# Optimization experiments

Hardware: AMD Instinct MI355X
Metric: run time of the kernel (lower is better)

## Reference

```python
import jax, jax.numpy as jnp
import numpy as np

E, S = 32768, 16
H, D_IN, EDGE_IN = 128, 128, 16
N_SRC, N_DST = 20000, 5000
HEADS, LAYERS, NUM_CLASS = 8, 2, 10
DH = H // HEADS


def _layer_norm(x, g, b, eps=1e-5):
    mu = jnp.mean(x, axis=-1, keepdims=True)
    var = jnp.mean((x - mu) ** 2, axis=-1, keepdims=True)
    return (x - mu) * jax.lax.rsqrt(var + eps) * g + b


def _encoder(e, e_mask, Wqkv, bqkv, Wo, bo, ln1_g, ln1_b, W1, b1, W2, b2, ln2_g, ln2_b):
    # e: [E,S,H]; e_mask: [E,S], True = padding. Post-norm encoder (PyTorch default).
    neg = jnp.float32(-1e9)
    for l in range(LAYERS):
        qkv = e @ Wqkv[l] + bqkv[l]                      # [E,S,3H]
        q, k, v = jnp.split(qkv, 3, axis=-1)
        q = q.reshape(E, S, HEADS, DH)
        k = k.reshape(E, S, HEADS, DH)
        v = v.reshape(E, S, HEADS, DH)
        scores = jnp.einsum('eqhd,ekhd->ehqk', q, k) / np.float32(np.sqrt(DH))
        scores = jnp.where(e_mask[:, None, None, :], neg, scores)
        attn = jax.nn.softmax(scores, axis=-1)
        ctx = jnp.einsum('ehqk,ekhd->eqhd', attn, v).reshape(E, S, H)
        e = _layer_norm(e + (ctx @ Wo[l] + bo[l]), ln1_g[l], ln1_b[l])
        ff = jax.nn.relu(e @ W1[l] + b1[l]) @ W2[l] + b2[l]
        e = _layer_norm(e + ff, ln2_g[l], ln2_b[l])
    return e


def _forward(node_features, edge_features, seq_times, subg_norm,
             W_ein, b_ein, enc_Wqkv, enc_bqkv, enc_Wo, enc_bo, enc_ln1_g, enc_ln1_b,
             enc_W1, enc_b1, enc_W2, enc_b2, enc_ln2_g, enc_ln2_b,
             W_eout, b_eout, W_node, b_node, W_fc, b_fc,
             e_len, e_mask, src_ids, dst_ids, layer_nid):
    h = node_features                                             # [N_src, D_IN]
    self_h = h[layer_nid]                                         # [N_dst, D_IN]
    self_h_tmp = jnp.concatenate([self_h, jnp.zeros((N_DST, H), h.dtype)], axis=1) @ W_eout + b_eout
    # message_func: per-edge sequence -> embed -> transformer -> pool -> concat with src h
    e = jnp.concatenate([edge_features, seq_times[..., None]], axis=-1)  # [E,S,EDGE_IN]
    e = jax.nn.relu(e @ W_ein + b_ein)                                   # [E,S,H]
    e = _encoder(e, e_mask, enc_Wqkv, enc_bqkv, enc_Wo, enc_bo,
                 enc_ln1_g, enc_ln1_b, enc_W1, enc_b1, enc_W2, enc_b2, enc_ln2_g, enc_ln2_b)
    valid = (~e_mask).astype(e.dtype)[..., None]
    e = jnp.sum(e * valid, axis=1) / e_len.astype(e.dtype)[:, None]      # masked mean pool [E,H]
    m = jax.nn.relu(jnp.concatenate([h[src_ids], e], axis=1) @ W_eout + b_eout)  # [E,H]
    h_agg = jax.ops.segment_sum(m, dst_ids, num_segments=N_DST)          # ragged mailbox sum
    hh = (h_agg - self_h_tmp) * subg_norm                                # NodeUpdate (train branch)
    z = jax.nn.relu(jnp.concatenate([self_h, hh], axis=1) @ W_node + b_node)
    return z @ W_fc + b_fc                                               # [N_dst, NUM_CLASS]


def setup_inputs() -> dict:
    key = jax.random.key(0)
    ks = jax.random.split(key, 32)
    inp = {}
    inp['node_features'] = jax.random.normal(ks[0], (N_SRC, D_IN), jnp.float32)
    inp['edge_features'] = jax.random.normal(ks[1], (E, S, EDGE_IN - 1), jnp.float32)
    inp['seq_times'] = jax.random.uniform(ks[2], (E, S), jnp.float32)
    e_len = jax.random.randint(ks[3], (E,), 1, S + 1).astype(jnp.int32)
    inp['e_len'] = e_len
    inp['e_mask'] = jnp.arange(S, dtype=jnp.int32)[None, :] >= e_len[:, None]  # True = pad
    inp['src_ids'] = jax.random.randint(ks[4], (E,), 0, N_SRC).astype(jnp.int32)
    inp['dst_ids'] = jax.random.randint(ks[5], (E,), 0, N_DST).astype(jnp.int32)
    inp['layer_nid'] = jax.random.randint(ks[6], (N_DST,), 0, N_SRC).astype(jnp.int32)
    inp['subg_norm'] = jax.random.uniform(ks[7], (N_DST, 1), jnp.float32, minval=0.01, maxval=1.0)

    def lin(k, fi, fo):
        return jax.random.normal(k, (fi, fo), jnp.float32) / np.float32(np.sqrt(fi))

    inp['W_ein'] = lin(ks[8], EDGE_IN, H); inp['b_ein'] = jnp.zeros((H,), jnp.float32)
    inp['enc_Wqkv'] = jax.random.normal(ks[9], (LAYERS, H, 3 * H), jnp.float32) / np.float32(np.sqrt(H))
    inp['enc_bqkv'] = jnp.zeros((LAYERS, 3 * H), jnp.float32)
    inp['enc_Wo'] = jax.random.normal(ks[10], (LAYERS, H, H), jnp.float32) / np.float32(np.sqrt(H))
    inp['enc_bo'] = jnp.zeros((LAYERS, H), jnp.float32)
    inp['enc_ln1_g'] = jnp.ones((LAYERS, H), jnp.float32); inp['enc_ln1_b'] = jnp.zeros((LAYERS, H), jnp.float32)
    inp['enc_W1'] = jax.random.normal(ks[11], (LAYERS, H, H), jnp.float32) / np.float32(np.sqrt(H))
    inp['enc_b1'] = jnp.zeros((LAYERS, H), jnp.float32)
    inp['enc_W2'] = jax.random.normal(ks[12], (LAYERS, H, H), jnp.float32) / np.float32(np.sqrt(H))
    inp['enc_b2'] = jnp.zeros((LAYERS, H), jnp.float32)
    inp['enc_ln2_g'] = jnp.ones((LAYERS, H), jnp.float32); inp['enc_ln2_b'] = jnp.zeros((LAYERS, H), jnp.float32)
    inp['W_eout'] = lin(ks[13], D_IN + H, H); inp['b_eout'] = jnp.zeros((H,), jnp.float32)
    inp['W_node'] = lin(ks[14], D_IN + H, H); inp['b_node'] = jnp.zeros((H,), jnp.float32)
    inp['W_fc'] = lin(ks[15], H, NUM_CLASS); inp['b_fc'] = jnp.zeros((NUM_CLASS,), jnp.float32)
    return inp


def reference(node_features, edge_features, seq_times, e_len, e_mask, src_ids, dst_ids,
              layer_nid, subg_norm, W_ein, b_ein, enc_Wqkv, enc_bqkv, enc_Wo, enc_bo,
              enc_ln1_g, enc_ln1_b, enc_W1, enc_b1, enc_W2, enc_b2, enc_ln2_g, enc_ln2_b,
              W_eout, b_eout, W_node, b_node, W_fc, b_fc):
    return _forward(node_features, edge_features, seq_times, subg_norm,
                    W_ein, b_ein, enc_Wqkv, enc_bqkv, enc_Wo, enc_bo, enc_ln1_g, enc_ln1_b,
                    enc_W1, enc_b1, enc_W2, enc_b2, enc_ln2_g, enc_ln2_b,
                    W_eout, b_eout, W_node, b_node, W_fc, b_fc,
                    e_len, e_mask, src_ids, dst_ids, layer_nid)
```

## Files before the change

### kernel.cpp

```cpp
#include <hip/hip_runtime.h>

typedef __attribute__((ext_vector_type(8))) short bf16x8;
typedef __attribute__((ext_vector_type(4))) float f32x4;

#define E_N      32768
#define N_DST_N  5000
#define NCLS     10

#define OFF_HAGG   0
#define OFF_POOL   2560000
#define OFF_WPACK  10948608

#define PK_QKV(l)  ((l) * 6144)
#define PK_WO(l)   (12288 + (l) * 2048)
#define PK_W1(l)   (16384 + (l) * 2048)
#define PK_W2(l)   (20480 + (l) * 2048)
#define PK_WEOUT   24576

#define QP 408
#define AP 136
#define EP 132

__device__ __forceinline__ unsigned short f2bf(float f) {
    unsigned int u = __float_as_uint(f);
    u += 0x7fffu + ((u >> 16) & 1u);
    return (unsigned short)(u >> 16);
}
__device__ __forceinline__ float bf2f(unsigned short u) {
    return __uint_as_float(((unsigned int)u) << 16);
}

__global__ void pack_weights(const float* __restrict__ Wqkv,
                             const float* __restrict__ Wo,
                             const float* __restrict__ W1,
                             const float* __restrict__ W2,
                             const float* __restrict__ W_eout,
                             unsigned short* __restrict__ wpack) {
    int gid = blockIdx.x * 256 + threadIdx.x;
    if (gid >= 229376) return;
    int id = gid;
    const float* src; int K, N, li;
    if (id < 98304)       { src = Wqkv + (id / 49152) * 49152; li = id % 49152; K = 128; N = 384; }
    else if (id < 131072) { id -= 98304;  src = Wo + (id / 16384) * 16384; li = id % 16384; K = 128; N = 128; }
    else if (id < 163840) { id -= 131072; src = W1 + (id / 16384) * 16384; li = id % 16384; K = 128; N = 128; }
    else if (id < 196608) { id -= 163840; src = W2 + (id / 16384) * 16384; li = id % 16384; K = 128; N = 128; }
    else                  { li = id - 196608; src = W_eout; K = 256; N = 128; }
    int j = li & 7, lane = (li >> 3) & 63, rest = li >> 9;
    int ks = K >> 5;
    int kk = rest % ks, t = rest / ks;
    int k = kk * 32 + ((lane >> 4) << 3) + j;
    int n = t * 16 + (lane & 15);
    wpack[gid] = f2bf(src[k * N + n]);
}

__global__ __launch_bounds__(256, 3) void edge_kernel(
    const float* __restrict__ edge_features,
    const float* __restrict__ seq_times,
    const int*   __restrict__ e_len,
    const float* __restrict__ W_ein, const float* __restrict__ b_ein,
    const float* __restrict__ bqkv,  const float* __restrict__ bo,
    const float* __restrict__ ln1_g, const float* __restrict__ ln1_b,
    const float* __restrict__ b1,    const float* __restrict__ b2,
    const float* __restrict__ ln2_g, const float* __restrict__ ln2_b,
    const unsigned short* __restrict__ wpack,
    unsigned short* __restrict__ pooled)
{
    __shared__ float e_f32[32][EP];
    __shared__ __align__(16) unsigned short a_bf[32][AP];
    __shared__ __align__(16) unsigned short qkv_bf[32][QP];
    __shared__ float x_lds[32][16];

    const int tid  = threadIdx.x;
    const int e0   = blockIdx.x * 2;
    const int lane = tid & 63;
    const int w    = tid >> 6;
    const int c16  = lane & 15;
    const int row4 = (lane >> 4) << 2;
    const int kblk = (lane >> 4) << 3;
    const int len0 = e_len[e0];
    const int len1 = e_len[e0 + 1];

#pragma unroll
    for (int idx = tid; idx < 512; idx += 256) {
        int e = idx >> 8, s = (idx >> 4) & 15, i = idx & 15;
        x_lds[e * 16 + s][i] = (i < 15) ? edge_features[(e0 + e) * 240 + s * 15 + i]
                                        : seq_times[(e0 + e) * 16 + s];
    }
    __syncthreads();

    {
        int c = tid & 127, er = (tid >> 7) * 16;
        float acc[16];
#pragma unroll
        for (int r = 0; r < 16; ++r) acc[r] = 0.f;
#pragma unroll
        for (int i = 0; i < 16; ++i) {
            float wt = W_ein[i * 128 + c];
#pragma unroll
            for (int r = 0; r < 16; ++r)
                acc[r] = fmaf(x_lds[er + r][i], wt, acc[r]);
        }
        float bv = b_ein[c];
#pragma unroll
        for (int r = 0; r < 16; ++r) {
            float v = fmaxf(acc[r] + bv, 0.f);
            e_f32[er + r][c] = v;
            a_bf[er + r][c]  = f2bf(v);
        }
    }
    __syncthreads();

    const bf16x8* WP = (const bf16x8*)wpack;

    for (int l = 0; l < 2; ++l) {
        {
            bf16x8 af[2][4];
#pragma unroll
            for (int rt = 0; rt < 2; ++rt)
#pragma unroll
                for (int kk = 0; kk < 4; ++kk)
                    af[rt][kk] = *(const bf16x8*)&a_bf[rt * 16 + c16][kk * 32 + kblk];
            const bf16x8* B = WP + PK_QKV(l);
#pragma unroll
            for (int half = 0; half < 2; ++half) {
                bf16x8 bq[3][4];
#pragma unroll
                for (int ti = 0; ti < 3; ++ti)
#pragma unroll
                    for (int kk = 0; kk < 4; ++kk)
                        bq[ti][kk] = B[((w * 6 + half * 3 + ti) * 4 + kk) * 64 + lane];
#pragma unroll
                for (int ti = 0; ti < 3; ++ti) {
                    int t = w * 6 + half * 3 + ti;
                    int seg = t >> 3;
                    int ldcol = seg * 136 + (t & 7) * 16 + c16;
                    float bias = bqkv[l * 384 + t * 16 + c16];
#pragma unroll
                    for (int rt = 0; rt < 2; ++rt) {
                        f32x4 acc = {0.f, 0.f, 0.f, 0.f};
#pragma unroll
                        for (int kk = 0; kk < 4; ++kk)
                            acc = __builtin_amdgcn_mfma_f32_16x16x32_bf16(
                                af[rt][kk], bq[ti][kk], acc, 0, 0, 0);
#pragma unroll
                        for (int r = 0; r < 4; ++r)
                            qkv_bf[rt * 16 + row4 + r][ldcol] = f2bf(acc[r] + bias);
                    }
                }
            }
        }
        __syncthreads();

        {
            int e  = tid >> 7;
            int hb = ((tid >> 4) & 7) * 16;
            int qq = tid & 15;
            int er = e * 16;
            int len = e ? len1 : len0;
            float qv[16];
            {
                bf16x8 v0 = *(const bf16x8*)&qkv_bf[er + qq][hb];
                bf16x8 v1 = *(const bf16x8*)&qkv_bf[er + qq][hb + 8];
#pragma unroll
                for (int j = 0; j < 8; ++j) {
                    qv[j]     = bf2f((unsigned short)v0[j]);
                    qv[8 + j] = bf2f((unsigned short)v1[j]);
                }
            }
            float sc[16];
            float mx = -1e30f;
#pragma unroll
            for (int kk = 0; kk < 16; ++kk) {
                bf16x8 k0 = *(const bf16x8*)&qkv_bf[er + kk][136 + hb];
                bf16x8 k1 = *(const bf16x8*)&qkv_bf[er + kk][136 + hb + 8];
                float s = 0.f;
#pragma unroll
                for (int j = 0; j < 8; ++j) {
                    s = fmaf(qv[j],     bf2f((unsigned short)k0[j]), s);
                    s = fmaf(qv[8 + j], bf2f((unsigned short)k1[j]), s);
                }
                s *= 0.25f;
                sc[kk] = s;
                mx = fmaxf(mx, (kk < len) ? s : -1e30f);
            }
            float sum = 0.f;
#pragma unroll
            for (int kk = 0; kk < 16; ++kk) {
                float p = (kk < len) ? __expf(sc[kk] - mx) : 0.f;
                sc[kk] = p;
                sum += p;
            }
            float inv = 1.f / sum;
            float ctx[16];
#pragma unroll
            for (int d = 0; d < 16; ++d) ctx[d] = 0.f;
#pragma unroll
            for (int kk = 0; kk < 16; ++kk) {
                float p = sc[kk] * inv;
                bf16x8 v0 = *(const bf16x8*)&qkv_bf[er + kk][272 + hb];
                bf16x8 v1 = *(const bf16x8*)&qkv_bf[er + kk][272 + hb + 8];
#pragma unroll
                for (int j = 0; j < 8; ++j) {
                    ctx[j]     = fmaf(p, bf2f((unsigned short)v0[j]), ctx[j]);
                    ctx[8 + j] = fmaf(p, bf2f((unsigned short)v1[j]), ctx[8 + j]);
                }
            }
            bf16x8 o0, o1;
#pragma unroll
            for (int j = 0; j < 8; ++j) {
                o0[j] = (short)f2bf(ctx[j]);
                o1[j] = (short)f2bf(ctx[8 + j]);
            }
            __syncthreads();
            *(bf16x8*)&a_bf[er + qq][hb]     = o0;
            *(bf16x8*)&a_bf[er + qq][hb + 8] = o1;
        }
        __syncthreads();

        {
            bf16x8 af[2][4];
#pragma unroll
            for (int rt = 0; rt < 2; ++rt)
#pragma unroll
                for (int kk = 0; kk < 4; ++kk)
                    af[rt][kk] = *(const bf16x8*)&a_bf[rt * 16 + c16][kk * 32 + kblk];
            const bf16x8* B = WP + PK_WO(l);
            bf16x8 bw[2][4];
#pragma unroll
            for (int ti = 0; ti < 2; ++ti)
#pragma unroll
                for (int kk = 0; kk < 4; ++kk)
                    bw[ti][kk] = B[((w * 2 + ti) * 4 + kk) * 64 + lane];
#pragma unroll
            for (int ti = 0; ti < 2; ++ti) {
                int col = (w * 2 + ti) * 16 + c16;
                float bias = bo[l * 128 + col];
#pragma unroll
                for (int rt = 0; rt < 2; ++rt) {
                    f32x4 acc = {0.f, 0.f, 0.f, 0.f};
#pragma unroll
                    for (int kk = 0; kk < 4; ++kk)
                        acc = __builtin_amdgcn_mfma_f32_16x16x32_bf16(
                            af[rt][kk], bw[ti][kk], acc, 0, 0, 0);
#pragma unroll
                    for (int r = 0; r < 4; ++r)
                        e_f32[rt * 16 + row4 + r][col] += acc[r] + bias;
                }
            }
        }
        __syncthreads();

        {
            const float* g = ln1_g + l * 128;
            const float* b = ln1_b + l * 128;
            int r = tid >> 3, j = tid & 7;
            float vals[16];
#pragma unroll
            for (int m = 0; m < 16; ++m) vals[m] = e_f32[r][j + 8 * m];
            float s = 0.f;
#pragma unroll
            for (int m = 0; m < 16; ++m) s += vals[m];
            s += __shfl_xor(s, 1); s += __shfl_xor(s, 2); s += __shfl_xor(s, 4);
            float mu = s * (1.f / 128.f);
            float v = 0.f;
#pragma unroll
            for (int m = 0; m < 16; ++m) { float d = vals[m] - mu; v = fmaf(d, d, v); }
            v += __shfl_xor(v, 1); v += __shfl_xor(v, 2); v += __shfl_xor(v, 4);
            float inv = rsqrtf(v * (1.f / 128.f) + 1e-5f);
#pragma unroll
            for (int m = 0; m < 16; ++m) {
                int col = j + 8 * m;
                float y = (vals[m] - mu) * inv * g[col] + b[col];
                e_f32[r][col] = y;
                a_bf[r][col]  = f2bf(y);
            }
        }
        __syncthreads();

        {
            bf16x8 af[2][4];
#pragma unroll
            for (int rt = 0; rt < 2; ++rt)
#pragma unroll
                for (int kk = 0; kk < 4; ++kk)
                    af[rt][kk] = *(const bf16x8*)&a_bf[rt * 16 + c16][kk * 32 + kblk];
            const bf16x8* B = WP + PK_W1(l);
            bf16x8 bw[2][4];
#pragma unroll
            for (int ti = 0; ti < 2; ++ti)
#pragma unroll
                for (int kk = 0; kk < 4; ++kk)
                    bw[ti][kk] = B[((w * 2 + ti) * 4 + kk) * 64 + lane];
            f32x4 acc2[2][2];
#pragma unroll
            for (int ti = 0; ti < 2; ++ti)
#pragma unroll
                for (int rt = 0; rt < 2; ++rt) {
                    f32x4 acc = {0.f, 0.f, 0.f, 0.f};
#pragma unroll
                    for (int kk = 0; kk < 4; ++kk)
                        acc = __builtin_amdgcn_mfma_f32_16x16x32_bf16(
                            af[rt][kk], bw[ti][kk], acc, 0, 0, 0);
                    acc2[ti][rt] = acc;
                }
            __syncthreads();
#pragma unroll
            for (int ti = 0; ti < 2; ++ti) {
                int col = (w * 2 + ti) * 16 + c16;
                float bias = b1[l * 128 + col];
#pragma unroll
                for (int rt = 0; rt < 2; ++rt)
#pragma unroll
                    for (int r = 0; r < 4; ++r)
                        a_bf[rt * 16 + row4 + r][col] =
                            f2bf(fmaxf(acc2[ti][rt][r] + bias, 0.f));
            }
        }
        __syncthreads();

        {
            bf16x8 af[2][4];
#pragma unroll
            for (int rt = 0; rt < 2; ++rt)
#pragma unroll
                for (int kk = 0; kk < 4; ++kk)
                    af[rt][kk] = *(const bf16x8*)&a_bf[rt * 16 + c16][kk * 32 + kblk];
            const bf16x8* B = WP + PK_W2(l);
            bf16x8 bw[2][4];
#pragma unroll
            for (int ti = 0; ti < 2; ++ti)
#pragma unroll
                for (int kk = 0; kk < 4; ++kk)
                    bw[ti][kk] = B[((w * 2 + ti) * 4 + kk) * 64 + lane];
#pragma unroll
            for (int ti = 0; ti < 2; ++ti) {
                int col = (w * 2 + ti) * 16 + c16;
                float bias = b2[l * 128 + col];
#pragma unroll
                for (int rt = 0; rt < 2; ++rt) {
                    f32x4 acc = {0.f, 0.f, 0.f, 0.f};
#pragma unroll
                    for (int kk = 0; kk < 4; ++kk)
                        acc = __builtin_amdgcn_mfma_f32_16x16x32_bf16(
                            af[rt][kk], bw[ti][kk], acc, 0, 0, 0);
#pragma unroll
                    for (int r = 0; r < 4; ++r)
                        e_f32[rt * 16 + row4 + r][col] += acc[r] + bias;
                }
            }
        }
        __syncthreads();

        {
            const float* g = ln2_g + l * 128;
            const float* b = ln2_b + l * 128;
            int r = tid >> 3, j = tid & 7;
            float vals[16];
#pragma unroll
            for (int m = 0; m < 16; ++m) vals[m] = e_f32[r][j + 8 * m];
            float s = 0.f;
#pragma unroll
            for (int m = 0; m < 16; ++m) s += vals[m];
            s += __shfl_xor(s, 1); s += __shfl_xor(s, 2); s += __shfl_xor(s, 4);
            float mu = s * (1.f / 128.f);
            float v = 0.f;
#pragma unroll
            for (int m = 0; m < 16; ++m) { float d = vals[m] - mu; v = fmaf(d, d, v); }
            v += __shfl_xor(v, 1); v += __shfl_xor(v, 2); v += __shfl_xor(v, 4);
            float inv = rsqrtf(v * (1.f / 128.f) + 1e-5f);
#pragma unroll
            for (int m = 0; m < 16; ++m) {
                int col = j + 8 * m;
                float y = (vals[m] - mu) * inv * g[col] + b[col];
                e_f32[r][col] = y;
                a_bf[r][col]  = f2bf(y);
            }
        }
        __syncthreads();
    }

    {
        int e = tid >> 7, c = tid & 127;
        int len = e ? len1 : len0;
        float s = 0.f;
#pragma unroll
        for (int ss = 0; ss < 16; ++ss)
            s += (ss < len) ? e_f32[e * 16 + ss][c] : 0.f;
        pooled[(e0 + e) * 128 + c] = f2bf(s / (float)len);
    }
}

__global__ __launch_bounds__(256) void edge_out_kernel(
    const float* __restrict__ node_features,
    const int* __restrict__ src_ids, const int* __restrict__ dst_ids,
    const unsigned short* __restrict__ pooled,
    const unsigned short* __restrict__ wpack,
    const float* __restrict__ b_eout,
    float* __restrict__ h_agg)
{
    __shared__ __align__(16) unsigned short a2[16][264];
    __shared__ int dst_s[16];
    const int tid = threadIdx.x, lane = tid & 63, w = tid >> 6;
    const int e0 = blockIdx.x * 16;

    {
        int r = tid >> 4, cm = tid & 15;
        int e = e0 + r;
        int src = src_ids[e];
#pragma unroll
        for (int m = 0; m < 8; ++m) {
            int col = cm + 16 * m;
            a2[r][col] = f2bf(node_features[src * 128 + col]);
        }
#pragma unroll
        for (int m = 0; m < 8; ++m) {
            int col = cm + 16 * m;
            a2[r][128 + col] = pooled[e * 128 + col];
        }
        if (tid < 16) dst_s[tid] = dst_ids[e0 + tid];
    }
    __syncthreads();

    const int c16 = lane & 15, row4 = (lane >> 4) << 2, kblk = (lane >> 4) << 3;
    bf16x8 af[8];
#pragma unroll
    for (int kk = 0; kk < 8; ++kk)
        af[kk] = *(const bf16x8*)&a2[c16][kk * 32 + kblk];
    const bf16x8* B = (const bf16x8*)wpack + PK_WEOUT;
#pragma unroll
    for (int ti = 0; ti < 2; ++ti) {
        int t = w * 2 + ti;
        f32x4 acc = {0.f, 0.f, 0.f, 0.f};
#pragma unroll
        for (int kk = 0; kk < 8; ++kk)
            acc = __builtin_amdgcn_mfma_f32_16x16x32_bf16(
                af[kk], B[(t * 8 + kk) * 64 + lane], acc, 0, 0, 0);
        int col = t * 16 + c16;
        float bias = b_eout[col];
#pragma unroll
        for (int r = 0; r < 4; ++r) {
            int row = row4 + r;
            float v = fmaxf(acc[r] + bias, 0.f);
            atomicAdd(&h_agg[dst_s[row] * 128 + col], v);
        }
    }
}

__global__ __launch_bounds__(128) void node_kernel(
    const float* __restrict__ node_features,
    const int*   __restrict__ layer_nid,
    const float* __restrict__ subg_norm,
    const float* __restrict__ h_agg,
    const float* __restrict__ W_eout, const float* __restrict__ b_eout,
    const float* __restrict__ W_node, const float* __restrict__ b_node,
    const float* __restrict__ W_fc,   const float* __restrict__ b_fc,
    float* __restrict__ out)
{
    __shared__ float sh[128];
    __shared__ float hh[128];
    __shared__ float z[128];

    const int n   = blockIdx.x;
    const int tid = threadIdx.x;
    const int nid = layer_nid[n];
    const float norm = subg_norm[n];

    sh[tid] = node_features[nid * 128 + tid];
    __syncthreads();

    float acc = 0.f;
#pragma unroll 4
    for (int k = 0; k < 128; ++k)
        acc = fmaf(sh[k], W_eout[k * 128 + tid], acc);
    acc += b_eout[tid];
    hh[tid] = (h_agg[n * 128 + tid] - acc) * norm;
    __syncthreads();

    float za = 0.f;
#pragma unroll 4
    for (int k = 0; k < 128; ++k)
        za = fmaf(sh[k], W_node[k * 128 + tid], za);
#pragma unroll 4
    for (int k = 0; k < 128; ++k)
        za = fmaf(hh[k], W_node[(128 + k) * 128 + tid], za);
    za += b_node[tid];
    z[tid] = fmaxf(za, 0.f);
    __syncthreads();

    if (tid < NCLS) {
        float o = 0.f;
#pragma unroll 4
        for (int k = 0; k < 128; ++k)
            o = fmaf(z[k], W_fc[k * NCLS + tid], o);
        out[n * NCLS + tid] = o + b_fc[tid];
    }
}


extern "C" void kernel_launch(void* const* d_in, const int* in_sizes, int n_in,
                              void* d_out, int out_size, void* d_ws, size_t ws_size,
                              hipStream_t stream) {
    const float* node_features = (const float*)d_in[0];
    const float* edge_features = (const float*)d_in[1];
    const float* seq_times     = (const float*)d_in[2];
    const int*   e_len         = (const int*)d_in[3];
    const int*   src_ids       = (const int*)d_in[5];
    const int*   dst_ids       = (const int*)d_in[6];
    const int*   layer_nid     = (const int*)d_in[7];
    const float* subg_norm     = (const float*)d_in[8];
    const float* W_ein  = (const float*)d_in[9];
    const float* b_ein  = (const float*)d_in[10];
    const float* Wqkv   = (const float*)d_in[11];
    const float* bqkv   = (const float*)d_in[12];
    const float* Wo     = (const float*)d_in[13];
    const float* bo     = (const float*)d_in[14];
    const float* ln1_g  = (const float*)d_in[15];
    const float* ln1_b  = (const float*)d_in[16];
    const float* W1     = (const float*)d_in[17];
    const float* b1     = (const float*)d_in[18];
    const float* W2     = (const float*)d_in[19];
    const float* b2     = (const float*)d_in[20];
    const float* ln2_g  = (const float*)d_in[21];
    const float* ln2_b  = (const float*)d_in[22];
    const float* W_eout = (const float*)d_in[23];
    const float* b_eout = (const float*)d_in[24];
    const float* W_node = (const float*)d_in[25];
    const float* b_node = (const float*)d_in[26];
    const float* W_fc   = (const float*)d_in[27];
    const float* b_fc   = (const float*)d_in[28];

    float*          h_agg  = (float*)((char*)d_ws + OFF_HAGG);
    unsigned short* pooled = (unsigned short*)((char*)d_ws + OFF_POOL);
    unsigned short* wpack  = (unsigned short*)((char*)d_ws + OFF_WPACK);

    pack_weights<<<896, 256, 0, stream>>>(Wqkv, Wo, W1, W2, W_eout, wpack);
    hipMemsetAsync(h_agg, 0, (size_t)N_DST_N * 128 * sizeof(float), stream);

    edge_kernel<<<E_N / 2, 256, 0, stream>>>(
        edge_features, seq_times, e_len,
        W_ein, b_ein, bqkv, bo, ln1_g, ln1_b, b1, b2, ln2_g, ln2_b,
        wpack, pooled);

    edge_out_kernel<<<E_N / 16, 256, 0, stream>>>(
        node_features, src_ids, dst_ids, pooled, wpack, b_eout, h_agg);

    node_kernel<<<N_DST_N, 128, 0, stream>>>(
        node_features, layer_nid, subg_norm, h_agg,
        W_eout, b_eout, W_node, b_node, W_fc, b_fc, (float*)d_out);
}
```

Baseline: 888.5 us.

## Move edge encoder attention and input projection to MFMA, keep residual in registers

The per-edge encoder kernel now computes the input embedding and both attention products (QK^T and PV) with bf16 MFMA instructions instead of scalar FMA loops. It stores V transposed and K separately in LDS, and keeps the fp32 residual stream in registers rather than an LDS fp32 buffer. LayerNorm becomes a register-based two-pass reduction through small LDS partial-sum arrays, and mean pooling reads directly from registers. The intent is less LDS traffic and capacity, fewer barriers and scalar FLOPs, and higher occupancy. In exchange, attention probabilities and the input are rounded to bf16, variance uses E[x^2]-mu^2, and half the lanes in the attention MFMAs carry zero padding.

```diff
diff --git a/kernel.cpp b/kernel.cpp
--- a/kernel.cpp
+++ b/kernel.cpp
@@ -1,6 +1,7 @@
 #include <hip/hip_runtime.h>
 
 typedef __attribute__((ext_vector_type(8))) short bf16x8;
+typedef __attribute__((ext_vector_type(4))) short s16x4;
 typedef __attribute__((ext_vector_type(4))) float f32x4;
 
 #define E_N      32768
@@ -16,18 +17,12 @@
 #define PK_W1(l)   (16384 + (l) * 2048)
 #define PK_W2(l)   (20480 + (l) * 2048)
 #define PK_WEOUT   24576
-
-#define QP 408
-#define AP 136
-#define EP 132
+#define PK_WEIN    28672
 
 __device__ __forceinline__ unsigned short f2bf(float f) {
     unsigned int u = __float_as_uint(f);
     u += 0x7fffu + ((u >> 16) & 1u);
     return (unsigned short)(u >> 16);
-}
-__device__ __forceinline__ float bf2f(unsigned short u) {
-    return __uint_as_float(((unsigned int)u) << 16);
 }
 
 __global__ void pack_weights(const float* __restrict__ Wqkv,
@@ -35,9 +30,18 @@
                              const float* __restrict__ W1,
                              const float* __restrict__ W2,
                              const float* __restrict__ W_eout,
+                             const float* __restrict__ W_ein,
                              unsigned short* __restrict__ wpack) {
     int gid = blockIdx.x * 256 + threadIdx.x;
-    if (gid >= 229376) return;
+    if (gid >= 233472) return;
+    if (gid >= 229376) {
+        int li = gid - 229376;
+        int j = li & 7, lane = (li >> 3) & 63, t = li >> 9;
+        int k = ((lane >> 4) << 3) + j;
+        int n = t * 16 + (lane & 15);
+        wpack[gid] = (k < 16) ? f2bf(W_ein[k * 128 + n]) : (unsigned short)0;
+        return;
+    }
     int id = gid;
     const float* src; int K, N, li;
     if (id < 98304)       { src = Wqkv + (id / 49152) * 49152; li = id % 49152; K = 128; N = 384; }
@@ -53,11 +57,65 @@
     wpack[gid] = f2bf(src[k * N + n]);
 }
 
+__device__ __forceinline__ void layer_norm_reg(
+    float res[2][2][4],
+    const float gcol[2], const float bcol[2],
+    unsigned short (*a_bf)[136],
+    float (*psum)[4], float (*psq)[4],
+    int w, int c16, int row4)
+{
+    float sv[2][4], qv[2][4];
+#pragma unroll
+    for (int rt = 0; rt < 2; ++rt)
+#pragma unroll
+        for (int r = 0; r < 4; ++r) {
+            float x0 = res[rt][0][r], x1 = res[rt][1][r];
+            float s = x0 + x1;
+            float q = x0 * x0 + x1 * x1;
+#pragma unroll
+            for (int d = 1; d < 16; d <<= 1) {
+                s += __shfl_xor(s, d);
+                q += __shfl_xor(q, d);
+            }
+            sv[rt][r] = s; qv[rt][r] = q;
+        }
+    if (c16 == 0) {
+#pragma unroll
+        for (int rt = 0; rt < 2; ++rt)
+#pragma unroll
+            for (int r = 0; r < 4; ++r) {
+                int row = rt * 16 + row4 + r;
+                psum[row][w] = sv[rt][r];
+                psq[row][w]  = qv[rt][r];
+            }
+    }
+    __syncthreads();
+#pragma unroll
+    for (int rt = 0; rt < 2; ++rt)
+#pragma unroll
+        for (int r = 0; r < 4; ++r) {
+            int row = rt * 16 + row4 + r;
+            float4 S = *(const float4*)&psum[row][0];
+            float4 Q = *(const float4*)&psq[row][0];
+            float sum = (S.x + S.y) + (S.z + S.w);
+            float sq  = (Q.x + Q.y) + (Q.z + Q.w);
+            float mu  = sum * (1.f / 128.f);
+            float var = sq * (1.f / 128.f) - mu * mu;
+            float inv = rsqrtf(var + 1e-5f);
+#pragma unroll
+            for (int ti = 0; ti < 2; ++ti) {
+                float y = (res[rt][ti][r] - mu) * inv * gcol[ti] + bcol[ti];
+                res[rt][ti][r] = y;
+                a_bf[row][w * 32 + ti * 16 + c16] = f2bf(y);
+            }
+        }
+}
+
 __global__ __launch_bounds__(256, 3) void edge_kernel(
     const float* __restrict__ edge_features,
     const float* __restrict__ seq_times,
     const int*   __restrict__ e_len,
-    const float* __restrict__ W_ein, const float* __restrict__ b_ein,
+    const float* __restrict__ b_ein,
     const float* __restrict__ bqkv,  const float* __restrict__ bo,
     const float* __restrict__ ln1_g, const float* __restrict__ ln1_b,
     const float* __restrict__ b1,    const float* __restrict__ b2,
@@ -65,52 +123,74 @@
     const unsigned short* __restrict__ wpack,
     unsigned short* __restrict__ pooled)
 {
-    __shared__ float e_f32[32][EP];
-    __shared__ __align__(16) unsigned short a_bf[32][AP];
-    __shared__ __align__(16) unsigned short qkv_bf[32][QP];
-    __shared__ float x_lds[32][16];
+    __shared__ __align__(16) unsigned short a_bf[32][136];
+    __shared__ __align__(16) unsigned short k_bf[32][136];
+    __shared__ __align__(16) unsigned short vT[2][128][24];
+    __shared__ __align__(16) unsigned short x_bf[32][40];
+    __shared__ __align__(16) float psum[32][4];
+    __shared__ __align__(16) float psq[32][4];
 
     const int tid  = threadIdx.x;
     const int e0   = blockIdx.x * 2;
     const int lane = tid & 63;
     const int w    = tid >> 6;
     const int c16  = lane & 15;
-    const int row4 = (lane >> 4) << 2;
-    const int kblk = (lane >> 4) << 3;
+    const int g    = lane >> 4;
+    const int row4 = g << 2;
+    const int kblk = g << 3;
     const int len0 = e_len[e0];
     const int len1 = e_len[e0 + 1];
-
-#pragma unroll
-    for (int idx = tid; idx < 512; idx += 256) {
-        int e = idx >> 8, s = (idx >> 4) & 15, i = idx & 15;
-        x_lds[e * 16 + s][i] = (i < 15) ? edge_features[(e0 + e) * 240 + s * 15 + i]
-                                        : seq_times[(e0 + e) * 16 + s];
-    }
-    __syncthreads();
+    const f32x4 z4 = {0.f, 0.f, 0.f, 0.f};
+
+    float res[2][2][4];
+
+    float lnG[2][2][2], lnB[2][2][2];
+#pragma unroll
+    for (int l = 0; l < 2; ++l)
+#pragma unroll
+        for (int ti = 0; ti < 2; ++ti) {
+            int col = w * 32 + ti * 16 + c16;
+            lnG[l][0][ti] = ln1_g[l * 128 + col];
+            lnB[l][0][ti] = ln1_b[l * 128 + col];
+            lnG[l][1][ti] = ln2_g[l * 128 + col];
+            lnB[l][1][ti] = ln2_b[l * 128 + col];
+        }
+
+    for (int idx = tid; idx < 1024; idx += 256) {
+        int r = idx >> 5, cc = idx & 31;
+        int e = r >> 4, s = r & 15;
+        float v = 0.f;
+        if (cc < 15)       v = edge_features[(e0 + e) * 240 + s * 15 + cc];
+        else if (cc == 15) v = seq_times[(e0 + e) * 16 + s];
+        x_bf[r][cc] = f2bf(v);
+    }
+    __syncthreads();
+
+    const bf16x8* WP = (const bf16x8*)wpack;
 
     {
-        int c = tid & 127, er = (tid >> 7) * 16;
-        float acc[16];
-#pragma unroll
-        for (int r = 0; r < 16; ++r) acc[r] = 0.f;
-#pragma unroll
-        for (int i = 0; i < 16; ++i) {
-            float wt = W_ein[i * 128 + c];
-#pragma unroll
-            for (int r = 0; r < 16; ++r)
-                acc[r] = fmaf(x_lds[er + r][i], wt, acc[r]);
-        }
-        float bv = b_ein[c];
-#pragma unroll
-        for (int r = 0; r < 16; ++r) {
-            float v = fmaxf(acc[r] + bv, 0.f);
-            e_f32[er + r][c] = v;
-            a_bf[er + r][c]  = f2bf(v);
-        }
-    }
-    __syncthreads();
-
-    const bf16x8* WP = (const bf16x8*)wpack;
+        bf16x8 axf[2];
+#pragma unroll
+        for (int rt = 0; rt < 2; ++rt)
+            axf[rt] = *(const bf16x8*)&x_bf[rt * 16 + c16][kblk];
+#pragma unroll
+        for (int ti = 0; ti < 2; ++ti) {
+            bf16x8 bw = WP[PK_WEIN + (2 * w + ti) * 64 + lane];
+            int col = (2 * w + ti) * 16 + c16;
+            float bias = b_ein[col];
+#pragma unroll
+            for (int rt = 0; rt < 2; ++rt) {
+                f32x4 acc = __builtin_amdgcn_mfma_f32_16x16x32_bf16(axf[rt], bw, z4, 0, 0, 0);
+#pragma unroll
+                for (int r = 0; r < 4; ++r) {
+                    float v = fmaxf(acc[r] + bias, 0.f);
+                    res[rt][ti][r] = v;
+                    a_bf[rt * 16 + row4 + r][col] = f2bf(v);
+                }
+            }
+        }
+    }
+    __syncthreads();
 
     for (int l = 0; l < 2; ++l) {
         {
@@ -120,100 +200,96 @@
 #pragma unroll
                 for (int kk = 0; kk < 4; ++kk)
                     af[rt][kk] = *(const bf16x8*)&a_bf[rt * 16 + c16][kk * 32 + kblk];
+            __syncthreads();
             const bf16x8* B = WP + PK_QKV(l);
 #pragma unroll
-            for (int half = 0; half < 2; ++half) {
-                bf16x8 bq[3][4];
-#pragma unroll
-                for (int ti = 0; ti < 3; ++ti)
+            for (int seg = 0; seg < 3; ++seg) {
+                bf16x8 bq[2][4];
+#pragma unroll
+                for (int ti = 0; ti < 2; ++ti)
 #pragma unroll
                     for (int kk = 0; kk < 4; ++kk)
-                        bq[ti][kk] = B[((w * 6 + half * 3 + ti) * 4 + kk) * 64 + lane];
-#pragma unroll
-                for (int ti = 0; ti < 3; ++ti) {
-                    int t = w * 6 + half * 3 + ti;
-                    int seg = t >> 3;
-                    int ldcol = seg * 136 + (t & 7) * 16 + c16;
-                    float bias = bqkv[l * 384 + t * 16 + c16];
+                        bq[ti][kk] = B[((seg * 8 + 2 * w + ti) * 4 + kk) * 64 + lane];
+#pragma unroll
+                for (int ti = 0; ti < 2; ++ti) {
+                    int col = (2 * w + ti) * 16 + c16;
+                    float bias = bqkv[l * 384 + seg * 128 + col];
 #pragma unroll
                     for (int rt = 0; rt < 2; ++rt) {
-                        f32x4 acc = {0.f, 0.f, 0.f, 0.f};
+                        f32x4 acc = z4;
 #pragma unroll
                         for (int kk = 0; kk < 4; ++kk)
                             acc = __builtin_amdgcn_mfma_f32_16x16x32_bf16(
                                 af[rt][kk], bq[ti][kk], acc, 0, 0, 0);
-#pragma unroll
-                        for (int r = 0; r < 4; ++r)
-                            qkv_bf[rt * 16 + row4 + r][ldcol] = f2bf(acc[r] + bias);
+                        if (seg == 0) {
+#pragma unroll
+                            for (int r = 0; r < 4; ++r)
+                                a_bf[rt * 16 + row4 + r][col] = f2bf(acc[r] + bias);
+                        } else if (seg == 1) {
+#pragma unroll
+                            for (int r = 0; r < 4; ++r)
+                                k_bf[rt * 16 + row4 + r][col] = f2bf(acc[r] + bias);
+                        } else {
+                            s16x4 pk;
+#pragma unroll
+                            for (int r = 0; r < 4; ++r)
+                                pk[r] = (short)f2bf(acc[r] + bias);
+                            *(s16x4*)&vT[rt][col][row4] = pk;
+                        }
                     }
                 }
             }
         }
         __syncthreads();
 
-        {
-            int e  = tid >> 7;
-            int hb = ((tid >> 4) & 7) * 16;
-            int qq = tid & 15;
+#pragma unroll
+        for (int i = 0; i < 4; ++i) {
+            int pp = w * 4 + i;
+            int e  = pp >> 3;
+            int hb = (pp & 7) * 16;
             int er = e * 16;
             int len = e ? len1 : len0;
-            float qv[16];
-            {
-                bf16x8 v0 = *(const bf16x8*)&qkv_bf[er + qq][hb];
-                bf16x8 v1 = *(const bf16x8*)&qkv_bf[er + qq][hb + 8];
-#pragma unroll
-                for (int j = 0; j < 8; ++j) {
-                    qv[j]     = bf2f((unsigned short)v0[j]);
-                    qv[8 + j] = bf2f((unsigned short)v1[j]);
-                }
-            }
-            float sc[16];
-            float mx = -1e30f;
-#pragma unroll
-            for (int kk = 0; kk < 16; ++kk) {
-                bf16x8 k0 = *(const bf16x8*)&qkv_bf[er + kk][136 + hb];
-                bf16x8 k1 = *(const bf16x8*)&qkv_bf[er + kk][136 + hb + 8];
-                float s = 0.f;
-#pragma unroll
-                for (int j = 0; j < 8; ++j) {
-                    s = fmaf(qv[j],     bf2f((unsigned short)k0[j]), s);
-                    s = fmaf(qv[8 + j], bf2f((unsigned short)k1[j]), s);
-                }
-                s *= 0.25f;
-                sc[kk] = s;
-                mx = fmaxf(mx, (kk < len) ? s : -1e30f);
-            }
-            float sum = 0.f;
-#pragma unroll
-            for (int kk = 0; kk < 16; ++kk) {
-                float p = (kk < len) ? __expf(sc[kk] - mx) : 0.f;
-                sc[kk] = p;
-                sum += p;
-            }
-            float inv = 1.f / sum;
-            float ctx[16];
-#pragma unroll
-            for (int d = 0; d < 16; ++d) ctx[d] = 0.f;
-#pragma unroll
-            for (int kk = 0; kk < 16; ++kk) {
-                float p = sc[kk] * inv;
-                bf16x8 v0 = *(const bf16x8*)&qkv_bf[er + kk][272 + hb];
-                bf16x8 v1 = *(const bf16x8*)&qkv_bf[er + kk][272 + hb + 8];
-#pragma unroll
-                for (int j = 0; j < 8; ++j) {
-                    ctx[j]     = fmaf(p, bf2f((unsigned short)v0[j]), ctx[j]);
-                    ctx[8 + j] = fmaf(p, bf2f((unsigned short)v1[j]), ctx[8 + j]);
-                }
-            }
-            bf16x8 o0, o1;
-#pragma unroll
-            for (int j = 0; j < 8; ++j) {
-                o0[j] = (short)f2bf(ctx[j]);
-                o1[j] = (short)f2bf(ctx[8 + j]);
-            }
-            __syncthreads();
-            *(bf16x8*)&a_bf[er + qq][hb]     = o0;
-            *(bf16x8*)&a_bf[er + qq][hb + 8] = o1;
+            bf16x8 kf = {0,0,0,0,0,0,0,0};
+            bf16x8 qf = {0,0,0,0,0,0,0,0};
+            bf16x8 vf = {0,0,0,0,0,0,0,0};
+            if (lane < 32) {
+                kf = *(const bf16x8*)&k_bf[er + c16][hb + kblk];
+                qf = *(const bf16x8*)&a_bf[er + c16][hb + kblk];
+                vf = *(const bf16x8*)&vT[e][hb + c16][kblk];
+            }
+            f32x4 st = __builtin_amdgcn_mfma_f32_16x16x32_bf16(kf, qf, z4, 0, 0, 0);
+            float sv[4]; float mx = -1e30f;
+#pragma unroll
+            for (int r = 0; r < 4; ++r) {
+                sv[r] = st[r] * 0.25f;
+                if (4 * g + r < len) mx = fmaxf(mx, sv[r]);
+            }
+            mx = fmaxf(mx, __shfl_xor(mx, 16));
+            mx = fmaxf(mx, __shfl_xor(mx, 32));
+            float p[4]; float sum = 0.f;
+#pragma unroll
+            for (int r = 0; r < 4; ++r) {
+                float pe = (4 * g + r < len) ? __expf(sv[r] - mx) : 0.f;
+                p[r] = pe; sum += pe;
+            }
+            sum += __shfl_xor(sum, 16);
+            sum += __shfl_xor(sum, 32);
+            float inv = __fdividef(1.f, sum);
+            unsigned int own0 = (unsigned int)f2bf(p[0] * inv) | ((unsigned int)f2bf(p[1] * inv) << 16);
+            unsigned int own1 = (unsigned int)f2bf(p[2] * inv) | ((unsigned int)f2bf(p[3] * inv) << 16);
+            unsigned int t0a = (unsigned int)__shfl((int)own0, (lane + 16) & 63);
+            unsigned int t1a = (unsigned int)__shfl((int)own1, (lane + 16) & 63);
+            unsigned int t0b = (unsigned int)__shfl((int)own0, (lane + 32) & 63);
+            unsigned int t1b = (unsigned int)__shfl((int)own1, (lane + 32) & 63);
+            union { unsigned int u[4]; bf16x8 v; } pb;
+            if (g == 0)      { pb.u[0] = own0; pb.u[1] = own1; pb.u[2] = t0a; pb.u[3] = t1a; }
+            else if (g == 1) { pb.u[0] = t0a;  pb.u[1] = t1a;  pb.u[2] = t0b; pb.u[3] = t1b; }
+            else             { pb.u[0] = 0; pb.u[1] = 0; pb.u[2] = 0; pb.u[3] = 0; }
+            f32x4 ct = __builtin_amdgcn_mfma_f32_16x16x32_bf16(vf, pb.v, z4, 0, 0, 0);
+            s16x4 cpk;
+#pragma unroll
+            for (int r = 0; r < 4; ++r) cpk[r] = (short)f2bf(ct[r]);
+            *(s16x4*)&a_bf[er + c16][hb + 4 * g] = cpk;
         }
         __syncthreads();
 
@@ -230,51 +306,25 @@
             for (int ti = 0; ti < 2; ++ti)
 #pragma unroll
                 for (int kk = 0; kk < 4; ++kk)
-                    bw[ti][kk] = B[((w * 2 + ti) * 4 + kk) * 64 + lane];
+                    bw[ti][kk] = B[((2 * w + ti) * 4 + kk) * 64 + lane];
 #pragma unroll
             for (int ti = 0; ti < 2; ++ti) {
-                int col = (w * 2 + ti) * 16 + c16;
+                int col = (2 * w + ti) * 16 + c16;
                 float bias = bo[l * 128 + col];
 #pragma unroll
                 for (int rt = 0; rt < 2; ++rt) {
-                    f32x4 acc = {0.f, 0.f, 0.f, 0.f};
+                    f32x4 acc = z4;
 #pragma unroll
                     for (int kk = 0; kk < 4; ++kk)
                         acc = __builtin_amdgcn_mfma_f32_16x16x32_bf16(
                             af[rt][kk], bw[ti][kk], acc, 0, 0, 0);
 #pragma unroll
                     for (int r = 0; r < 4; ++r)
-                        e_f32[rt * 16 + row4 + r][col] += acc[r] + bias;
+                        res[rt][ti][r] += acc[r] + bias;
                 }
             }
         }
-        __syncthreads();
-
-        {
-            const float* g = ln1_g + l * 128;
-            const float* b = ln1_b + l * 128;
-            int r = tid >> 3, j = tid & 7;
-            float vals[16];
-#pragma unroll
-            for (int m = 0; m < 16; ++m) vals[m] = e_f32[r][j + 8 * m];
-            float s = 0.f;
-#pragma unroll
-            for (int m = 0; m < 16; ++m) s += vals[m];
-            s += __shfl_xor(s, 1); s += __shfl_xor(s, 2); s += __shfl_xor(s, 4);
-            float mu = s * (1.f / 128.f);
-            float v = 0.f;
-#pragma unroll
-            for (int m = 0; m < 16; ++m) { float d = vals[m] - mu; v = fmaf(d, d, v); }
-            v += __shfl_xor(v, 1); v += __shfl_xor(v, 2); v += __shfl_xor(v, 4);
-            float inv = rsqrtf(v * (1.f / 128.f) + 1e-5f);
-#pragma unroll
-            for (int m = 0; m < 16; ++m) {
-                int col = j + 8 * m;
-                float y = (vals[m] - mu) * inv * g[col] + b[col];
-                e_f32[r][col] = y;
-                a_bf[r][col]  = f2bf(y);
-            }
-        }
+        layer_norm_reg(res, lnG[l][0], lnB[l][0], a_bf, psum, psq, w, c16, row4);
         __syncthreads();
 
         {
@@ -290,13 +340,13 @@
             for (int ti = 0; ti < 2; ++ti)
 #pragma unroll
                 for (int kk = 0; kk < 4; ++kk)
-                    bw[ti][kk] = B[((w * 2 + ti) * 4 + kk) * 64 + lane];
+                    bw[ti][kk] = B[((2 * w + ti) * 4 + kk) * 64 + lane];
             f32x4 acc2[2][2];
 #pragma unroll
             for (int ti = 0; ti < 2; ++ti)
 #pragma unroll
                 for (int rt = 0; rt < 2; ++rt) {
-                    f32x4 acc = {0.f, 0.f, 0.f, 0.f};
+                    f32x4 acc = z4;
 #pragma unroll
                     for (int kk = 0; kk < 4; ++kk)
                         acc = __builtin_amdgcn_mfma_f32_16x16x32_bf16(
@@ -306,7 +356,7 @@
             __syncthreads();
 #pragma unroll
             for (int ti = 0; ti < 2; ++ti) {
-                int col = (w * 2 + ti) * 16 + c16;
+                int col = (2 * w + ti) * 16 + c16;
                 float bias = b1[l * 128 + col];
 #pragma unroll
                 for (int rt = 0; rt < 2; ++rt)
@@ -331,62 +381,43 @@
             for (int ti = 0; ti < 2; ++ti)
 #pragma unroll
                 for (int kk = 0; kk < 4; ++kk)
-                    bw[ti][kk] = B[((w * 2 + ti) * 4 + kk) * 64 + lane];
+                    bw[ti][kk] = B[((2 * w + ti) * 4 + kk) * 64 + lane];
 #pragma unroll
             for (int ti = 0; ti < 2; ++ti) {
-                int col = (w * 2 + ti) * 16 + c16;
+                int col = (2 * w + ti) * 16 + c16;
                 float bias = b2[l * 128 + col];
 #pragma unroll
                 for (int rt = 0; rt < 2; ++rt) {
-                    f32x4 acc = {0.f, 0.f, 0.f, 0.f};
+                    f32x4 acc = z4;
 #pragma unroll
                     for (int kk = 0; kk < 4; ++kk)
                         acc = __builtin_amdgcn_mfma_f32_16x16x32_bf16(
                             af[rt][kk], bw[ti][kk], acc, 0, 0, 0);
 #pragma unroll
                     for (int r = 0; r < 4; ++r)
-                        e_f32[rt * 16 + row4 + r][col] += acc[r] + bias;
+                        res[rt][ti][r] += acc[r] + bias;
                 }
             }
         }
+        layer_norm_reg(res, lnG[l][1], lnB[l][1], a_bf, psum, psq, w, c16, row4);
         __syncthreads();
-
-        {
-            const float* g = ln2_g + l * 128;
-            const float* b = ln2_b + l * 128;
-            int r = tid >> 3, j = tid & 7;
-            float vals[16];
-#pragma unroll
-            for (int m = 0; m < 16; ++m) vals[m] = e_f32[r][j + 8 * m];
+    }
+
+#pragma unroll
+    for (int rt = 0; rt < 2; ++rt) {
+        int len = rt ? len1 : len0;
+        float fln = (float)len;
+#pragma unroll
+        for (int ti = 0; ti < 2; ++ti) {
             float s = 0.f;
 #pragma unroll
-            for (int m = 0; m < 16; ++m) s += vals[m];
-            s += __shfl_xor(s, 1); s += __shfl_xor(s, 2); s += __shfl_xor(s, 4);
-            float mu = s * (1.f / 128.f);
-            float v = 0.f;
-#pragma unroll
-            for (int m = 0; m < 16; ++m) { float d = vals[m] - mu; v = fmaf(d, d, v); }
-            v += __shfl_xor(v, 1); v += __shfl_xor(v, 2); v += __shfl_xor(v, 4);
-            float inv = rsqrtf(v * (1.f / 128.f) + 1e-5f);
-#pragma unroll
-            for (int m = 0; m < 16; ++m) {
-                int col = j + 8 * m;
-                float y = (vals[m] - mu) * inv * g[col] + b[col];
-                e_f32[r][col] = y;
-                a_bf[r][col]  = f2bf(y);
-            }
-        }
-        __syncthreads();
-    }
-
-    {
-        int e = tid >> 7, c = tid & 127;
-        int len = e ? len1 : len0;
-        float s = 0.f;
-#pragma unroll
-        for (int ss = 0; ss < 16; ++ss)
-            s += (ss < len) ? e_f32[e * 16 + ss][c] : 0.f;
-        pooled[(e0 + e) * 128 + c] = f2bf(s / (float)len);
+            for (int r = 0; r < 4; ++r)
+                if (row4 + r < len) s += res[rt][ti][r];
+            s += __shfl_xor(s, 16);
+            s += __shfl_xor(s, 32);
+            if (lane < 16)
+                pooled[(e0 + rt) * 128 + w * 32 + ti * 16 + c16] = f2bf(s / fln);
+        }
     }
 }
 
@@ -533,12 +564,12 @@
     unsigned short* pooled = (unsigned short*)((char*)d_ws + OFF_POOL);
     unsigned short* wpack  = (unsigned short*)((char*)d_ws + OFF_WPACK);
 
-    pack_weights<<<896, 256, 0, stream>>>(Wqkv, Wo, W1, W2, W_eout, wpack);
+    pack_weights<<<912, 256, 0, stream>>>(Wqkv, Wo, W1, W2, W_eout, W_ein, wpack);
     hipMemsetAsync(h_agg, 0, (size_t)N_DST_N * 128 * sizeof(float), stream);
 
     edge_kernel<<<E_N / 2, 256, 0, stream>>>(
         edge_features, seq_times, e_len,
-        W_ein, b_ein, bqkv, bo, ln1_g, ln1_b, b1, b2, ln2_g, ln2_b,
+        b_ein, bqkv, bo, ln1_g, ln1_b, b1, b2, ln2_g, ln2_b,
         wpack, pooled);
 
     edge_out_kernel<<<E_N / 16, 256, 0, stream>>>(
```

Result: faster. 827.7 us (-6.8%).
